# Kernel tuning notes

Hardware: AMD Instinct MI355X
Metric: run time of the kernel (lower is better)

The kernel has to match this reference:

```python
import jax, jax.numpy as jnp
import numpy as np


def setup_inputs() -> dict:
    key = jax.random.key(0)
    k1, k2 = jax.random.split(key)
    B, S, H = 8, 2048, 1024
    lstm_output = jax.random.normal(k1, (B, S, H), dtype=jnp.float32)
    # xavier-uniform-like init for the bilinear weight
    limit = float(np.sqrt(6.0 / (H + H)))
    attention_weights = jax.random.uniform(k2, (H, H), dtype=jnp.float32, minval=-limit, maxval=limit)
    return {"lstm_output": lstm_output, "attention_weights": attention_weights}


def reference(lstm_output, attention_weights):
    # scores[b,i,j] = (x[b,i] @ W) . x[b,j]
    xw = jnp.einsum('bsh,hk->bsk', lstm_output, attention_weights)      # [B,S,H]
    scores = jnp.einsum('bsk,btk->bst', xw, lstm_output)                # [B,S,S]
    attn = jax.nn.softmax(scores, axis=-1)                              # [B,S,S]
    context = jnp.einsum('bst,bth->bsh', attn, lstm_output)             # [B,S,H]
    return (context, attn)
```

## Files before the change

### kernel.cpp

```cpp
#include <hip/hip_runtime.h>
#include <hip/hip_bf16.h>


#define BB 8
#define SS 2048
#define HH 1024

typedef __attribute__((ext_vector_type(8))) short bf16x8;
typedef __attribute__((ext_vector_type(4))) float f32x4;

__device__ __forceinline__ void async_load16(const void* gsrc, void* ldst) {
    typedef const unsigned int __attribute__((address_space(1)))* gp_t;
    typedef unsigned int __attribute__((address_space(3)))* lp_t;
    __builtin_amdgcn_global_load_lds((gp_t)gsrc, (lp_t)ldst, 16, 0, 0);
}

__device__ __forceinline__ unsigned short f2b(float f) {
    __hip_bfloat16 h = __float2bfloat16(f);
    return *(unsigned short*)&h;
}
__device__ __forceinline__ float b2f(unsigned short u) {
    __hip_bfloat16 h = *(__hip_bfloat16*)&u;
    return __bfloat162float(h);
}

__global__ __launch_bounds__(256) void split_x(const float* __restrict__ X,
                                               unsigned short* __restrict__ Xh,
                                               unsigned short* __restrict__ Xl) {
    const size_t i = ((size_t)blockIdx.x * 256 + threadIdx.x) * 8;
    float4 a = *(const float4*)(X + i);
    float4 b = *(const float4*)(X + i + 4);
    ushort4 h0, h1, l0, l1;
    float v, hf;
    v = a.x; h0.x = f2b(v); hf = b2f(h0.x); l0.x = f2b(v - hf);
    v = a.y; h0.y = f2b(v); hf = b2f(h0.y); l0.y = f2b(v - hf);
    v = a.z; h0.z = f2b(v); hf = b2f(h0.z); l0.z = f2b(v - hf);
    v = a.w; h0.w = f2b(v); hf = b2f(h0.w); l0.w = f2b(v - hf);
    v = b.x; h1.x = f2b(v); hf = b2f(h1.x); l1.x = f2b(v - hf);
    v = b.y; h1.y = f2b(v); hf = b2f(h1.y); l1.y = f2b(v - hf);
    v = b.z; h1.z = f2b(v); hf = b2f(h1.z); l1.z = f2b(v - hf);
    v = b.w; h1.w = f2b(v); hf = b2f(h1.w); l1.w = f2b(v - hf);
    *(ushort4*)(Xh + i) = h0; *(ushort4*)(Xh + i + 4) = h1;
    *(ushort4*)(Xl + i) = l0; *(ushort4*)(Xl + i + 4) = l1;
}

__global__ __launch_bounds__(256) void split_wT(const float* __restrict__ W,
                                                unsigned short* __restrict__ Th,
                                                unsigned short* __restrict__ Tl) {
    const int k0 = blockIdx.y * 64, n0 = blockIdx.x * 64;
    __shared__ float tile[64][65];
#pragma unroll
    for (int q = 0; q < 16; q++) {
        int idx = q * 256 + threadIdx.x;
        int r = idx >> 6, c = idx & 63;
        tile[r][c] = W[(size_t)(k0 + r) * HH + n0 + c];
    }
    __syncthreads();
#pragma unroll
    for (int q = 0; q < 16; q++) {
        int idx = q * 256 + threadIdx.x;
        int r = idx >> 6, c = idx & 63;
        float v = tile[c][r];
        unsigned short h = f2b(v);
        Th[(size_t)(n0 + r) * HH + k0 + c] = h;
        Tl[(size_t)(n0 + r) * HH + k0 + c] = f2b(v - b2f(h));
    }
}

#define STG_A(mh, kt, buf) do { \
        const size_t o_ = aOff + (size_t)(mh) * 64 * HH + (size_t)(kt) * 32; \
        async_load16(A_h + o_, (char*)lds + ((buf) * 32768 + (mh) * 4096) * 2 + wt16); \
        async_load16(A_l + o_, (char*)lds + ((buf) * 32768 + 8192 + (mh) * 4096) * 2 + wt16); \
    } while (0)
#define STG_B(nh, kt, buf) do { \
        const size_t o_ = bOff + (size_t)(nh) * 32 * HH + (size_t)(kt) * 32; \
        async_load16(B_h + o_, (char*)lds + ((buf) * 32768 + 16384 + (nh) * 4096) * 2 + wt16); \
        async_load16(B_l + o_, (char*)lds + ((buf) * 32768 + 24576 + (nh) * 4096) * 2 + wt16); \
    } while (0)
#define RD_A_H(mh, buf) do { \
        const int s0_ = (buf) * 32768 + ((mh) * 128 + wy * 64 + m16) * 32 + cs * 8; \
        _Pragma("unroll") for (int mi = 0; mi < 4; ++mi) \
            a_h[mi] = *(const bf16x8*)&lds[s0_ + mi * 512]; \
    } while (0)
#define RD_A_L(mh, buf) do { \
        const int s0_ = (buf) * 32768 + ((mh) * 128 + wy * 64 + m16) * 32 + cs * 8; \
        _Pragma("unroll") for (int mi = 0; mi < 4; ++mi) \
            a_l[mi] = *(const bf16x8*)&lds[8192 + s0_ + mi * 512]; \
    } while (0)
#define RD_B_H(nh, buf) do { \
        const int s0_ = (buf) * 32768 + ((nh) * 128 + wx * 32 + m16) * 32 + cs * 8; \
        _Pragma("unroll") for (int nj = 0; nj < 2; ++nj) \
            b_h[nh][nj] = *(const bf16x8*)&lds[16384 + s0_ + nj * 512]; \
    } while (0)
#define RD_B_L(nh, buf) do { \
        const int s0_ = (buf) * 32768 + ((nh) * 128 + wx * 32 + m16) * 32 + cs * 8; \
        _Pragma("unroll") for (int nj = 0; nj < 2; ++nj) \
            b_l[nh][nj] = *(const bf16x8*)&lds[24576 + s0_ + nj * 512]; \
    } while (0)
#define PASS_HH(mh) \
        _Pragma("unroll") for (int mi = 0; mi < 4; ++mi) \
        _Pragma("unroll") for (int nh = 0; nh < 2; ++nh) \
        _Pragma("unroll") for (int nj = 0; nj < 2; ++nj) \
            acc[mh][mi][nh][nj] = __builtin_amdgcn_mfma_f32_16x16x32_bf16(a_h[mi], b_h[nh][nj], acc[mh][mi][nh][nj], 0, 0, 0);
#define PASS_HL(mh) \
        _Pragma("unroll") for (int mi = 0; mi < 4; ++mi) \
        _Pragma("unroll") for (int nh = 0; nh < 2; ++nh) \
        _Pragma("unroll") for (int nj = 0; nj < 2; ++nj) \
            acc[mh][mi][nh][nj] = __builtin_amdgcn_mfma_f32_16x16x32_bf16(a_h[mi], b_l[nh][nj], acc[mh][mi][nh][nj], 0, 0, 0);
#define PASS_LH(mh) \
        _Pragma("unroll") for (int mi = 0; mi < 4; ++mi) \
        _Pragma("unroll") for (int nh = 0; nh < 2; ++nh) \
        _Pragma("unroll") for (int nj = 0; nj < 2; ++nj) \
            acc[mh][mi][nh][nj] = __builtin_amdgcn_mfma_f32_16x16x32_bf16(a_l[mi], b_h[nh][nj], acc[mh][mi][nh][nj], 0, 0, 0);

#define SPLIT3_2PH_BODY(A_h, A_l, B_h, B_l)                                         \
    __shared__ __align__(16) unsigned short lds[65536];                             \
    const int tid = threadIdx.x;                                                    \
    const int wave = tid >> 6, lane = tid & 63;                                     \
    const int m16 = lane & 15, quad = lane >> 4;                                    \
    const int wy = wave >> 2, wx = wave & 3;                                        \
    const int rP = tid >> 2;                                                        \
    const int kq = (tid & 3) ^ ((rP >> 1) & 3);                                     \
    const int cs = quad ^ ((m16 >> 1) & 3);                                         \
    const int wt16 = wave * 1024;                                                   \
    const int rowA_off = (rP & 63) + ((rP >> 6) << 7);                              \
    const int rowB_off = ((rP >> 5) << 6) + (rP & 31);                              \
    const size_t aOff = (size_t)(i0 + rowA_off) * HH + kq * 8;                      \
    const size_t bOff = (size_t)(j0 + rowB_off) * HH + kq * 8;                      \
    f32x4 acc[2][4][2][2] = {};                                                     \
    bf16x8 a_h[4], a_l[4], b_h[2][2], b_l[2][2];                                    \
    STG_A(0, 0, 0); STG_A(1, 0, 0);                                                 \
    STG_B(0, 0, 0); STG_B(1, 0, 0);                                                 \
    STG_B(0, 1, 1); STG_B(1, 1, 1);                                                 \
    asm volatile("s_waitcnt vmcnt(4)" ::: "memory");                                \
    __builtin_amdgcn_s_barrier();                                                   \
    RD_A_H(0, 0); RD_A_L(0, 0);                                                     \
    RD_B_H(0, 0); RD_B_L(0, 0); RD_B_H(1, 0); RD_B_L(1, 0);                         \
    for (int kt = 0; kt < 32; ++kt) {                                               \
        const int bufc = kt & 1, bufn = bufc ^ 1;                                   \
        const int ktA = kt < 31 ? kt + 1 : 31;                                      \
        const int ktB = kt < 30 ? kt + 2 : 31;                                      \
                                                                \
        STG_A(0, ktA, bufn);                                                        \
        STG_A(1, ktA, bufn);                                                        \
        asm volatile("s_waitcnt vmcnt(8)" ::: "memory");                            \
        __builtin_amdgcn_s_barrier();                                               \
        __builtin_amdgcn_sched_barrier(0);                                          \
        __builtin_amdgcn_s_setprio(1);                                              \
        PASS_HH(0)                                                                  \
        PASS_HL(0)                                                                  \
        __builtin_amdgcn_sched_barrier(0);                                          \
        RD_A_H(1, bufc);                                                            \
        __builtin_amdgcn_sched_barrier(0);                                          \
        PASS_LH(0)                                                                  \
        __builtin_amdgcn_s_setprio(0);                                              \
        __builtin_amdgcn_sched_barrier(0);                                          \
        RD_A_L(1, bufc);                                                            \
        __builtin_amdgcn_s_barrier();                                               \
                                                                \
        STG_B(0, ktB, bufc);                                                        \
        STG_B(1, ktB, bufc);                                                        \
        asm volatile("s_waitcnt vmcnt(4)" ::: "memory");                            \
        __builtin_amdgcn_s_barrier();                                               \
        __builtin_amdgcn_sched_barrier(0);                                          \
        __builtin_amdgcn_s_setprio(1);                                              \
        PASS_HH(1)                                                                  \
        PASS_HL(1)                                                                  \
        __builtin_amdgcn_sched_barrier(0);                                          \
        RD_B_L(0, bufn); RD_B_L(1, bufn); RD_A_H(0, bufn);                          \
        __builtin_amdgcn_sched_barrier(0);                                          \
        PASS_LH(1)                                                                  \
        __builtin_amdgcn_s_setprio(0);                                              \
        __builtin_amdgcn_sched_barrier(0);                                          \
        RD_B_H(0, bufn); RD_B_H(1, bufn); RD_A_L(0, bufn);                          \
        __builtin_amdgcn_s_barrier();                                               \
    }

__global__ __launch_bounds__(512, 2) void gemm_xw3_8p(const unsigned short* __restrict__ Ah,
                                                      const unsigned short* __restrict__ Al,
                                                      const unsigned short* __restrict__ Bh,
                                                      const unsigned short* __restrict__ Bl,
                                                      unsigned short* __restrict__ Ch,
                                                      unsigned short* __restrict__ Cl) {
    const int b = blockIdx.z;
    const int i0 = blockIdx.y * 256, j0 = blockIdx.x * 256;
    const unsigned short* A_h = Ah + (size_t)b * SS * HH;
    const unsigned short* A_l = Al + (size_t)b * SS * HH;
    const unsigned short* B_h = Bh;
    const unsigned short* B_l = Bl;

    SPLIT3_2PH_BODY(A_h, A_l, B_h, B_l)

    unsigned short* ChB = Ch + (size_t)b * SS * HH;
    unsigned short* ClB = Cl + (size_t)b * SS * HH;
#pragma unroll
    for (int mh = 0; mh < 2; ++mh)
#pragma unroll
        for (int mi = 0; mi < 4; ++mi)
#pragma unroll
            for (int nh = 0; nh < 2; ++nh)
#pragma unroll
                for (int nj = 0; nj < 2; ++nj) {
                    const int row = i0 + wy * 128 + mh * 64 + mi * 16 + quad * 4;
                    const int col = j0 + wx * 64 + nh * 32 + nj * 16 + m16;
#pragma unroll
                    for (int reg = 0; reg < 4; ++reg) {
                        float v = acc[mh][mi][nh][nj][reg];
                        unsigned short h = f2b(v);
                        ChB[(size_t)(row + reg) * HH + col] = h;
                        ClB[(size_t)(row + reg) * HH + col] = f2b(v - b2f(h));
                    }
                }
}

__global__ __launch_bounds__(512, 2) void gemm_sc3_8p(const unsigned short* __restrict__ Ah,
                                                      const unsigned short* __restrict__ Al,
                                                      const unsigned short* __restrict__ Bh,
                                                      const unsigned short* __restrict__ Bl,
                                                      float* __restrict__ SC) {
    const int b = blockIdx.z;
    const int i0 = blockIdx.y * 256, j0 = blockIdx.x * 256;
    const unsigned short* A_h = Ah + (size_t)b * SS * HH;
    const unsigned short* A_l = Al + (size_t)b * SS * HH;
    const unsigned short* B_h = Bh + (size_t)b * SS * HH;
    const unsigned short* B_l = Bl + (size_t)b * SS * HH;

    SPLIT3_2PH_BODY(A_h, A_l, B_h, B_l)

    float* Cb = SC + (size_t)b * SS * SS;
#pragma unroll
    for (int mh = 0; mh < 2; ++mh)
#pragma unroll
        for (int mi = 0; mi < 4; ++mi)
#pragma unroll
            for (int nh = 0; nh < 2; ++nh)
#pragma unroll
                for (int nj = 0; nj < 2; ++nj) {
                    const int row = i0 + wy * 128 + mh * 64 + mi * 16 + quad * 4;
                    const int col = j0 + wx * 64 + nh * 32 + nj * 16 + m16;
#pragma unroll
                    for (int reg = 0; reg < 4; ++reg)
                        Cb[(size_t)(row + reg) * SS + col] = acc[mh][mi][nh][nj][reg];
                }
}

#undef STG_A
#undef STG_B
#undef RD_A_H
#undef RD_A_L
#undef RD_B_H
#undef RD_B_L
#undef PASS_HH
#undef PASS_HL
#undef PASS_LH
#undef SPLIT3_2PH_BODY

__global__ __launch_bounds__(256) void softmax_rows(float* __restrict__ P,
                                                    unsigned short* __restrict__ Pb) {
    const size_t row = blockIdx.x;
    float4* p4 = (float4*)(P + row * SS);
    const int tid = threadIdx.x;
    float4 v0 = p4[tid], v1 = p4[tid + 256];
    float m = fmaxf(fmaxf(fmaxf(v0.x, v0.y), fmaxf(v0.z, v0.w)),
                    fmaxf(fmaxf(v1.x, v1.y), fmaxf(v1.z, v1.w)));
#pragma unroll
    for (int off = 32; off; off >>= 1) m = fmaxf(m, __shfl_xor(m, off));
    __shared__ float red[4];
    const int wid = tid >> 6, lane = tid & 63;
    if (lane == 0) red[wid] = m;
    __syncthreads();
    m = fmaxf(fmaxf(red[0], red[1]), fmaxf(red[2], red[3]));
    v0.x = __expf(v0.x - m); v0.y = __expf(v0.y - m);
    v0.z = __expf(v0.z - m); v0.w = __expf(v0.w - m);
    v1.x = __expf(v1.x - m); v1.y = __expf(v1.y - m);
    v1.z = __expf(v1.z - m); v1.w = __expf(v1.w - m);
    float s = v0.x + v0.y + v0.z + v0.w + v1.x + v1.y + v1.z + v1.w;
#pragma unroll
    for (int off = 32; off; off >>= 1) s += __shfl_xor(s, off);
    __syncthreads();
    if (lane == 0) red[wid] = s;
    __syncthreads();
    s = red[0] + red[1] + red[2] + red[3];
    const float inv = 1.0f / s;
    v0.x *= inv; v0.y *= inv; v0.z *= inv; v0.w *= inv;
    v1.x *= inv; v1.y *= inv; v1.z *= inv; v1.w *= inv;
    p4[tid] = v0;
    p4[tid + 256] = v1;
    ushort4* b4 = (ushort4*)(Pb + row * SS);
    ushort4 u0 = { f2b(v0.x), f2b(v0.y), f2b(v0.z), f2b(v0.w) };
    ushort4 u1 = { f2b(v1.x), f2b(v1.y), f2b(v1.z), f2b(v1.w) };
    b4[tid] = u0;
    b4[tid + 256] = u1;
}

__global__ __launch_bounds__(256) void transpose_cvt(const float* __restrict__ X,
                                                     unsigned short* __restrict__ XT) {
    const int b = blockIdx.z;
    const int t0 = blockIdx.y * 64;
    const int h0 = blockIdx.x * 64;
    __shared__ float tile[64][65];
    const float* Xb = X + (size_t)b * SS * HH;
    unsigned short* Tb = XT + (size_t)b * HH * SS;
#pragma unroll
    for (int q = 0; q < 16; q++) {
        int idx = q * 256 + threadIdx.x;
        int r = idx >> 6, c = idx & 63;
        tile[r][c] = Xb[(size_t)(t0 + r) * HH + h0 + c];
    }
    __syncthreads();
#pragma unroll
    for (int q = 0; q < 16; q++) {
        int idx = q * 256 + threadIdx.x;
        int r = idx >> 6, c = idx & 63;
        Tb[(size_t)(h0 + r) * SS + t0 + c] = f2b(tile[c][r]);
    }
}

__global__ __launch_bounds__(512, 2) void gemm_ctx_8p(const unsigned short* __restrict__ Ab,
                                                      const unsigned short* __restrict__ Bt,
                                                      float* __restrict__ C) {
    const int b = blockIdx.z;
    const int i0 = blockIdx.y * 256, n0 = blockIdx.x * 256;
    const unsigned short* A = Ab + (size_t)b * SS * SS;
    const unsigned short* B = Bt + (size_t)b * HH * SS;

    __shared__ __align__(16) unsigned short lds[65536];

    const int tid = threadIdx.x;
    const int wave = tid >> 6, lane = tid & 63;
    const int m16 = lane & 15, quad = lane >> 4;
    const int m7 = m16 & 7;
    const int wy = wave >> 2, wx = wave & 3;
    const int rA8 = tid >> 3;
    const int c8 = (tid & 7) ^ (rA8 & 7);
    const int wt16 = wave * 1024;
    const int sl0 = (quad ^ m7) * 8;
    const int sl1 = ((quad + 4) ^ m7) * 8;

    const size_t aSrc = (size_t)(i0 + rA8) * SS + c8 * 8;
    const size_t bSrc = (size_t)(n0 + ((rA8 >> 5) << 6) + (rA8 & 31)) * SS + c8 * 8;

    f32x4 acc[2][4][2][2] = {};
    bf16x8 a[4][2], bb[2][2][2];

#define CSTG_A(mh, h, kt, buf) \
    async_load16(A + aSrc + (size_t)((mh) * 64 + (h) * 128) * SS + (size_t)(kt) * 64, \
                 (char*)lds + (buf) * 65536 + (mh) * 16384 + (h) * 8192 + wt16)
#define CSTG_B(nh, h, kt, buf) \
    async_load16(B + bSrc + (size_t)((h) * 128 + (nh) * 32) * SS + (size_t)(kt) * 64, \
                 (char*)lds + (buf) * 65536 + 32768 + (nh) * 16384 + (h) * 8192 + wt16)
#define CRD_A_S0(mh, buf) do { \
        const int r0_ = (buf) * 32768 + ((mh) * 128 + wy * 64 + m16) * 64; \
        _Pragma("unroll") for (int mi = 0; mi < 4; ++mi) \
            a[mi][0] = *(const bf16x8*)&lds[r0_ + mi * 1024 + sl0]; \
    } while (0)
#define CRD_A_S1(mh, buf) do { \
        const int r0_ = (buf) * 32768 + ((mh) * 128 + wy * 64 + m16) * 64; \
        _Pragma("unroll") for (int mi = 0; mi < 4; ++mi) \
            a[mi][1] = *(const bf16x8*)&lds[r0_ + mi * 1024 + sl1]; \
    } while (0)
#define CRD_B_S0(nh, buf) do { \
        const int r0_ = (buf) * 32768 + 16384 + (nh) * 8192 + (wx * 32 + m16) * 64; \
        _Pragma("unroll") for (int nj = 0; nj < 2; ++nj) \
            bb[nh][nj][0] = *(const bf16x8*)&lds[r0_ + nj * 1024 + sl0]; \
    } while (0)
#define CRD_B_S1(nh, buf) do { \
        const int r0_ = (buf) * 32768 + 16384 + (nh) * 8192 + (wx * 32 + m16) * 64; \
        _Pragma("unroll") for (int nj = 0; nj < 2; ++nj) \
            bb[nh][nj][1] = *(const bf16x8*)&lds[r0_ + nj * 1024 + sl1]; \
    } while (0)
#define CPASS0(mh) \
        _Pragma("unroll") for (int mi = 0; mi < 4; ++mi) \
        _Pragma("unroll") for (int nh = 0; nh < 2; ++nh) \
        _Pragma("unroll") for (int nj = 0; nj < 2; ++nj) \
            acc[mh][mi][nh][nj] = __builtin_amdgcn_mfma_f32_16x16x32_bf16(a[mi][0], bb[nh][nj][0], acc[mh][mi][nh][nj], 0, 0, 0);
#define CPASS1(mh) \
        _Pragma("unroll") for (int mi = 0; mi < 4; ++mi) \
        _Pragma("unroll") for (int nh = 0; nh < 2; ++nh) \
        _Pragma("unroll") for (int nj = 0; nj < 2; ++nj) \
            acc[mh][mi][nh][nj] = __builtin_amdgcn_mfma_f32_16x16x32_bf16(a[mi][1], bb[nh][nj][1], acc[mh][mi][nh][nj], 0, 0, 0);

    CSTG_A(0, 0, 0, 0); CSTG_A(0, 1, 0, 0);
    CSTG_A(1, 0, 0, 0); CSTG_A(1, 1, 0, 0);
    CSTG_B(0, 0, 0, 0); CSTG_B(0, 1, 0, 0);
    CSTG_B(1, 0, 0, 0); CSTG_B(1, 1, 0, 0);
    CSTG_B(0, 0, 1, 1); CSTG_B(0, 1, 1, 1);
    CSTG_B(1, 0, 1, 1); CSTG_B(1, 1, 1, 1);
    asm volatile("s_waitcnt vmcnt(4)" ::: "memory");
    __builtin_amdgcn_s_barrier();
    CRD_A_S0(0, 0); CRD_A_S1(0, 0);
    CRD_B_S0(0, 0); CRD_B_S1(0, 0); CRD_B_S0(1, 0); CRD_B_S1(1, 0);

    for (int kt = 0; kt < 32; ++kt) {
        const int bufc = kt & 1, bufn = bufc ^ 1;
        const int ktA = kt < 31 ? kt + 1 : 31;
        const int ktB = kt < 30 ? kt + 2 : 31;
        CSTG_A(0, 0, ktA, bufn); CSTG_A(0, 1, ktA, bufn);
        CSTG_A(1, 0, ktA, bufn); CSTG_A(1, 1, ktA, bufn);
        asm volatile("s_waitcnt vmcnt(8)" ::: "memory");
        __builtin_amdgcn_s_barrier();
        __builtin_amdgcn_sched_barrier(0);
        __builtin_amdgcn_s_setprio(1);
        CPASS0(0)
        __builtin_amdgcn_sched_barrier(0);
        CRD_A_S0(1, bufc);
        __builtin_amdgcn_sched_barrier(0);
        CPASS1(0)
        __builtin_amdgcn_s_setprio(0);
        __builtin_amdgcn_sched_barrier(0);
        CRD_A_S1(1, bufc);
        __builtin_amdgcn_s_barrier();
        CSTG_B(0, 0, ktB, bufc); CSTG_B(0, 1, ktB, bufc);
        CSTG_B(1, 0, ktB, bufc); CSTG_B(1, 1, ktB, bufc);
        asm volatile("s_waitcnt vmcnt(4)" ::: "memory");
        __builtin_amdgcn_s_barrier();
        __builtin_amdgcn_sched_barrier(0);
        __builtin_amdgcn_s_setprio(1);
        CPASS0(1)
        __builtin_amdgcn_sched_barrier(0);
        CRD_B_S0(0, bufn); CRD_B_S0(1, bufn); CRD_A_S0(0, bufn);
        __builtin_amdgcn_sched_barrier(0);
        CPASS1(1)
        __builtin_amdgcn_s_setprio(0);
        __builtin_amdgcn_sched_barrier(0);
        CRD_B_S1(0, bufn); CRD_B_S1(1, bufn); CRD_A_S1(0, bufn);
        __builtin_amdgcn_s_barrier();
    }

    float* Cb = C + (size_t)b * SS * HH;
#pragma unroll
    for (int mh = 0; mh < 2; ++mh)
#pragma unroll
        for (int mi = 0; mi < 4; ++mi)
#pragma unroll
            for (int nh = 0; nh < 2; ++nh)
#pragma unroll
                for (int nj = 0; nj < 2; ++nj) {
                    const int row = i0 + wy * 128 + mh * 64 + mi * 16 + quad * 4;
                    const int col = n0 + wx * 64 + nh * 32 + nj * 16 + m16;
#pragma unroll
                    for (int reg = 0; reg < 4; ++reg)
                        Cb[(size_t)(row + reg) * HH + col] = acc[mh][mi][nh][nj][reg];
                }
#undef CSTG_A
#undef CSTG_B
#undef CRD_A_S0
#undef CRD_A_S1
#undef CRD_B_S0
#undef CRD_B_S1
#undef CPASS0
#undef CPASS1
}

extern "C" void kernel_launch(void* const* d_in, const int* in_sizes, int n_in,
                              void* d_out, int out_size, void* d_ws, size_t ws_size,
                              hipStream_t stream) {
    const float* X = (const float*)d_in[0];
    const float* W = (const float*)d_in[1];
    float* ctx  = (float*)d_out;
    float* attn = ctx + (size_t)BB * SS * HH;

    char* ws = (char*)d_ws;
    unsigned short* x_hi  = (unsigned short*)ws;
    unsigned short* x_lo  = (unsigned short*)(ws + ((size_t)32 << 20));
    unsigned short* wt_hi = (unsigned short*)(ws + ((size_t)64 << 20));
    unsigned short* wt_lo = (unsigned short*)(ws + ((size_t)66 << 20));
    unsigned short* xT     = x_hi;
    unsigned short* attn_b = x_lo;

    unsigned short* xw_hi = (unsigned short*)d_out;
    unsigned short* xw_lo = xw_hi + (size_t)BB * SS * HH;

    dim3 blk(256);
    split_x <<<dim3(BB * SS * HH / (8 * 256)), blk, 0, stream>>>(X, x_hi, x_lo);
    split_wT<<<dim3(HH / 64, HH / 64), blk, 0, stream>>>(W, wt_hi, wt_lo);
    gemm_xw3_8p<<<dim3(HH / 256, SS / 256, BB), dim3(512), 0, stream>>>(x_hi, x_lo, wt_hi, wt_lo, xw_hi, xw_lo);
    gemm_sc3_8p<<<dim3(SS / 256, SS / 256, BB), dim3(512), 0, stream>>>(xw_hi, xw_lo, x_hi, x_lo, attn);
    transpose_cvt<<<dim3(HH / 64, SS / 64, BB), blk, 0, stream>>>(X, xT);
    softmax_rows <<<dim3(BB * SS), blk, 0, stream>>>(attn, attn_b);
    gemm_ctx_8p<<<dim3(HH / 256, SS / 256, BB), dim3(512), 0, stream>>>(attn_b, xT, ctx);
}
```

Measured before the change: 614.7 us.

## Swizzle GEMM tile order across XCDs, batch softmax rows, use nontemporal stores

Adds a block-index remap that groups consecutive tiles onto the same XCD (L & 7 interleave), so each XCD's L2 sees related A/B tiles in the three GEMMs. Softmax now handles two rows per 512-thread block, and its fp32 output and the context GEMM output are written with nontemporal stores to avoid polluting cache. The remap assumes the tile count is divisible by 8 and changes the scheduling order, which may alter L2 locality in either direction.

```diff
diff --git a/kernel.cpp b/kernel.cpp
--- a/kernel.cpp
+++ b/kernel.cpp
@@ -22,6 +22,16 @@
 __device__ __forceinline__ float b2f(unsigned short u) {
     __hip_bfloat16 h = *(__hip_bfloat16*)&u;
     return __bfloat162float(h);
+}
+
+__device__ __forceinline__ void swz_tile(int nx, int ny, int& tx, int& ty, int& tz) {
+    const int L = blockIdx.x + nx * (blockIdx.y + ny * blockIdx.z);
+    const int cpx = (nx * ny * BB) >> 3;
+    const int T = (L & 7) * cpx + (L >> 3);
+    tx = T % nx;
+    const int t2 = T / nx;
+    ty = t2 % ny;
+    tz = t2 / ny;
 }
 
 __global__ __launch_bounds__(256) void split_x(const float* __restrict__ X,
@@ -182,8 +192,9 @@
                                                       const unsigned short* __restrict__ Bl,
                                                       unsigned short* __restrict__ Ch,
                                                       unsigned short* __restrict__ Cl) {
-    const int b = blockIdx.z;
-    const int i0 = blockIdx.y * 256, j0 = blockIdx.x * 256;
+    int tx, ty, b;
+    swz_tile(gridDim.x, gridDim.y, tx, ty, b);
+    const int i0 = ty * 256, j0 = tx * 256;
     const unsigned short* A_h = Ah + (size_t)b * SS * HH;
     const unsigned short* A_l = Al + (size_t)b * SS * HH;
     const unsigned short* B_h = Bh;
@@ -218,8 +229,9 @@
                                                       const unsigned short* __restrict__ Bh,
                                                       const unsigned short* __restrict__ Bl,
                                                       float* __restrict__ SC) {
-    const int b = blockIdx.z;
-    const int i0 = blockIdx.y * 256, j0 = blockIdx.x * 256;
+    int tx, ty, b;
+    swz_tile(gridDim.x, gridDim.y, tx, ty, b);
+    const int i0 = ty * 256, j0 = tx * 256;
     const unsigned short* A_h = Ah + (size_t)b * SS * HH;
     const unsigned short* A_l = Al + (size_t)b * SS * HH;
     const unsigned short* B_h = Bh + (size_t)b * SS * HH;
@@ -255,21 +267,23 @@
 #undef PASS_LH
 #undef SPLIT3_2PH_BODY
 
-__global__ __launch_bounds__(256) void softmax_rows(float* __restrict__ P,
+__global__ __launch_bounds__(512) void softmax_rows(float* __restrict__ P,
                                                     unsigned short* __restrict__ Pb) {
-    const size_t row = blockIdx.x;
+    const int tid = threadIdx.x;
+    const int half = tid >> 8, t = tid & 255;
+    const size_t row = (size_t)blockIdx.x * 2 + half;
     float4* p4 = (float4*)(P + row * SS);
-    const int tid = threadIdx.x;
-    float4 v0 = p4[tid], v1 = p4[tid + 256];
+    float4 v0 = p4[t], v1 = p4[t + 256];
     float m = fmaxf(fmaxf(fmaxf(v0.x, v0.y), fmaxf(v0.z, v0.w)),
                     fmaxf(fmaxf(v1.x, v1.y), fmaxf(v1.z, v1.w)));
 #pragma unroll
     for (int off = 32; off; off >>= 1) m = fmaxf(m, __shfl_xor(m, off));
-    __shared__ float red[4];
+    __shared__ float red[8];
     const int wid = tid >> 6, lane = tid & 63;
+    const int rb = half << 2;
     if (lane == 0) red[wid] = m;
     __syncthreads();
-    m = fmaxf(fmaxf(red[0], red[1]), fmaxf(red[2], red[3]));
+    m = fmaxf(fmaxf(red[rb], red[rb + 1]), fmaxf(red[rb + 2], red[rb + 3]));
     v0.x = __expf(v0.x - m); v0.y = __expf(v0.y - m);
     v0.z = __expf(v0.z - m); v0.w = __expf(v0.w - m);
     v1.x = __expf(v1.x - m); v1.y = __expf(v1.y - m);
@@ -280,17 +294,17 @@
     __syncthreads();
     if (lane == 0) red[wid] = s;
     __syncthreads();
-    s = red[0] + red[1] + red[2] + red[3];
+    s = red[rb] + red[rb + 1] + red[rb + 2] + red[rb + 3];
     const float inv = 1.0f / s;
     v0.x *= inv; v0.y *= inv; v0.z *= inv; v0.w *= inv;
     v1.x *= inv; v1.y *= inv; v1.z *= inv; v1.w *= inv;
-    p4[tid] = v0;
-    p4[tid + 256] = v1;
+    __builtin_nontemporal_store(*(f32x4*)&v0, (f32x4*)(p4 + t));
+    __builtin_nontemporal_store(*(f32x4*)&v1, (f32x4*)(p4 + t + 256));
     ushort4* b4 = (ushort4*)(Pb + row * SS);
     ushort4 u0 = { f2b(v0.x), f2b(v0.y), f2b(v0.z), f2b(v0.w) };
     ushort4 u1 = { f2b(v1.x), f2b(v1.y), f2b(v1.z), f2b(v1.w) };
-    b4[tid] = u0;
-    b4[tid + 256] = u1;
+    b4[t] = u0;
+    b4[t + 256] = u1;
 }
 
 __global__ __launch_bounds__(256) void transpose_cvt(const float* __restrict__ X,
@@ -319,8 +333,9 @@
 __global__ __launch_bounds__(512, 2) void gemm_ctx_8p(const unsigned short* __restrict__ Ab,
                                                       const unsigned short* __restrict__ Bt,
                                                       float* __restrict__ C) {
-    const int b = blockIdx.z;
-    const int i0 = blockIdx.y * 256, n0 = blockIdx.x * 256;
+    int tx, ty, b;
+    swz_tile(gridDim.x, gridDim.y, tx, ty, b);
+    const int i0 = ty * 256, n0 = tx * 256;
     const unsigned short* A = Ab + (size_t)b * SS * SS;
     const unsigned short* B = Bt + (size_t)b * HH * SS;
 
@@ -440,7 +455,8 @@
                     const int col = n0 + wx * 64 + nh * 32 + nj * 16 + m16;
 #pragma unroll
                     for (int reg = 0; reg < 4; ++reg)
-                        Cb[(size_t)(row + reg) * HH + col] = acc[mh][mi][nh][nj][reg];
+                        __builtin_nontemporal_store(acc[mh][mi][nh][nj][reg],
+                                                    &Cb[(size_t)(row + reg) * HH + col]);
                 }
 #undef CSTG_A
 #undef CSTG_B
@@ -477,6 +493,6 @@
     gemm_xw3_8p<<<dim3(HH / 256, SS / 256, BB), dim3(512), 0, stream>>>(x_hi, x_lo, wt_hi, wt_lo, xw_hi, xw_lo);
     gemm_sc3_8p<<<dim3(SS / 256, SS / 256, BB), dim3(512), 0, stream>>>(xw_hi, xw_lo, x_hi, x_lo, attn);
     transpose_cvt<<<dim3(HH / 64, SS / 64, BB), blk, 0, stream>>>(X, xT);
-    softmax_rows <<<dim3(BB * SS), blk, 0, stream>>>(attn, attn_b);
+    softmax_rows <<<dim3(BB * SS / 2), dim3(512), 0, stream>>>(attn, attn_b);
     gemm_ctx_8p<<<dim3(HH / 256, SS / 256, BB), dim3(512), 0, stream>>>(attn_b, xT, ctx);
 }
```

New measurement: 607.5 us, median of 3. About the same (-1.2%).
